# Optimization experiments

Hardware: AMD Instinct MI355X
Metric: run time of the kernel (lower is better)

## Reference

```python
import jax, jax.numpy as jnp
import numpy as np

MU = 0.5
SMALL_MASS_CUTOFF = 1e-10
NP_PART = 2_000_000
W = 8            # linear hex stencil, 2^3 nodes per particle
DIM = 3
NC = 2_097_152   # 128^3 grid cells
NS = 200_000     # selected boundary (level-set) nodes


def setup_inputs() -> dict:
    key = jax.random.key(0)
    k0, k1, k2, k3, k4, k5 = jax.random.split(key, 6)
    mass_stack = jax.random.uniform(k0, (NP_PART,), dtype=jnp.float32)
    shapef_grad_stack = jax.random.normal(k1, (NP_PART, W, DIM), dtype=jnp.float32)
    cnode_ids = jax.random.randint(k2, (NP_PART, W), 0, NC, dtype=jnp.int32)
    node_moment_nt = jax.random.normal(k3, (NC, DIM), dtype=jnp.float32)
    node_mass = jax.random.uniform(k4, (NC,), dtype=jnp.float32)
    id_stack = jnp.arange(NS, dtype=jnp.int32)  # unique selected node ids
    velocity_stack = jax.random.normal(k5, (NS, DIM), dtype=jnp.float32)
    return {
        "mass_stack": mass_stack,
        "shapef_grad_stack": shapef_grad_stack,
        "cnode_ids": cnode_ids,
        "node_moment_nt": node_moment_nt,
        "node_mass": node_mass,
        "id_stack": id_stack,
        "velocity_stack": velocity_stack,
    }


def reference(mass_stack, shapef_grad_stack, cnode_ids, node_moment_nt,
              node_mass, id_stack, velocity_stack):
    dim = velocity_stack.shape[-1]
    nc = node_mass.shape[0]

    # ---- P2G: accumulate mass-weighted shape-function gradients into grid normals
    # normal[c] += shapef_grad[p, w, :dim] * mass[p] for every (p, w) -> c = cnode_ids[p, w]
    contrib = shapef_grad_stack * mass_stack[:, None, None]           # [Np, W, dim]
    normal_stack = jax.ops.segment_sum(contrib.reshape(-1, dim),
                                       cnode_ids.reshape(-1),
                                       num_segments=nc)               # [NC, dim]

    # ---- per selected node friction update (vectorized over NS)
    normal = normal_stack[id_stack]          # [NS, dim]
    moment_nt = node_moment_nt[id_stack]     # [NS, dim]
    mass = node_mass[id_stack]               # [NS]

    valid = mass > SMALL_MASS_CUTOFF
    inv_mass = jnp.where(valid, 1.0 / jnp.where(valid, mass, 1.0), 0.0)
    vel_nt = moment_nt * inv_mass[:, None]   # cond(mass>cutoff, m/mass, 0)

    nnorm = jnp.sqrt(jnp.sum(normal * normal, axis=-1, keepdims=True))
    nrm_ok = valid[:, None] & (nnorm > 0)
    normal_hat = jnp.where(nrm_ok, normal / jnp.where(nnorm > 0, nnorm, 1.0), 0.0)

    delta_vel = vel_nt - velocity_stack                                # [NS, dim]
    dvn = jnp.sum(delta_vel * normal_hat, axis=-1)                     # [NS]

    cross = jnp.cross(delta_vel, normal_hat)                           # [NS, 3]
    cnorm = jnp.sqrt(jnp.sum(cross * cross, axis=-1))                  # [NS]
    omega = jnp.where((cnorm > 0)[:, None],
                      cross / jnp.where(cnorm > 0, cnorm, 1.0)[:, None], 0.0)
    mu_prime = jnp.minimum(MU, cnorm / jnp.where(dvn != 0, dvn, 1.0))  # only used when dvn>0
    tangent = normal_hat + mu_prime[:, None] * jnp.cross(normal_hat, omega)

    apply_fric = (dvn > 0.0)[:, None]
    new_vel_nt = jnp.where(apply_fric, vel_nt - dvn[:, None] * tangent, vel_nt)
    levelset_moment = new_vel_nt * mass[:, None]                       # [NS, dim]

    # ---- scatter-set back into the grid moment field
    return node_moment_nt.at[id_stack].set(levelset_moment)
```

## Files before the change

kernel.cpp:

```cpp
#include <hip/hip_runtime.h>


#define MU_F 0.5f
#define SMALL_MASS_CUTOFF 1e-10f

__global__ void build_mask_kernel(const int* __restrict__ id_stack, int ns,
                                  unsigned int* __restrict__ mask,
                                  float* __restrict__ acc) {
    int i = blockIdx.x * blockDim.x + threadIdx.x;
    if (i >= ns) return;
    int id = id_stack[i];
    atomicOr(&mask[id >> 5], 1u << (id & 31));
    size_t b = (size_t)id * 3;
    acc[b + 0] = 0.0f;
    acc[b + 1] = 0.0f;
    acc[b + 2] = 0.0f;
}

template <int LOG2W>
__global__ void p2g_kernel(const float* __restrict__ mass_stack,
                           const float* __restrict__ grad,
                           const int*   __restrict__ ids,
                           const unsigned int* __restrict__ mask,
                           float* __restrict__ acc,
                           int npairs) {
    int pair = blockIdx.x * blockDim.x + threadIdx.x;
    if (pair >= npairs) return;
    int id = ids[pair];
    unsigned int w = mask[(unsigned)id >> 5];
    if (w & (1u << (id & 31))) {
        float m = mass_stack[pair >> LOG2W];
        const float* g = grad + (size_t)pair * 3;
        float gx = g[0], gy = g[1], gz = g[2];
        size_t b = (size_t)id * 3;
        unsafeAtomicAdd(&acc[b + 0], gx * m);
        unsafeAtomicAdd(&acc[b + 1], gy * m);
        unsafeAtomicAdd(&acc[b + 2], gz * m);
    }
}

__global__ void p2g_kernel_generic(const float* __restrict__ mass_stack,
                                   const float* __restrict__ grad,
                                   const int*   __restrict__ ids,
                                   const unsigned int* __restrict__ mask,
                                   float* __restrict__ acc,
                                   int npairs, int W) {
    int pair = blockIdx.x * blockDim.x + threadIdx.x;
    if (pair >= npairs) return;
    int id = ids[pair];
    unsigned int w = mask[(unsigned)id >> 5];
    if (w & (1u << (id & 31))) {
        float m = mass_stack[pair / W];
        const float* g = grad + (size_t)pair * 3;
        size_t b = (size_t)id * 3;
        unsafeAtomicAdd(&acc[b + 0], g[0] * m);
        unsafeAtomicAdd(&acc[b + 1], g[1] * m);
        unsafeAtomicAdd(&acc[b + 2], g[2] * m);
    }
}

__global__ void friction_kernel(const int*   __restrict__ id_stack,
                                const float* __restrict__ velocity,
                                const float* __restrict__ node_mass,
                                const float* __restrict__ node_moment,
                                const float* __restrict__ acc,
                                float* __restrict__ out,
                                int ns) {
    int i = blockIdx.x * blockDim.x + threadIdx.x;
    if (i >= ns) return;
    int id = id_stack[i];
    size_t b = (size_t)id * 3;

    float nx = acc[b + 0], ny = acc[b + 1], nz = acc[b + 2];
    float mass = node_mass[id];
    float mx = node_moment[b + 0], my = node_moment[b + 1], mz = node_moment[b + 2];

    bool valid = mass > SMALL_MASS_CUTOFF;
    float inv_mass = valid ? 1.0f / mass : 0.0f;
    float vx = mx * inv_mass, vy = my * inv_mass, vz = mz * inv_mass;

    float nn = sqrtf(nx * nx + ny * ny + nz * nz);
    bool ok = valid && (nn > 0.0f);
    float hx = 0.0f, hy = 0.0f, hz = 0.0f;
    if (ok) { float r = 1.0f / nn; hx = nx * r; hy = ny * r; hz = nz * r; }

    size_t vb = (size_t)i * 3;
    float dvx = vx - velocity[vb + 0];
    float dvy = vy - velocity[vb + 1];
    float dvz = vz - velocity[vb + 2];
    float dvn = dvx * hx + dvy * hy + dvz * hz;

    float ox = vx, oy = vy, oz = vz;
    if (dvn > 0.0f) {
        float cx = dvy * hz - dvz * hy;
        float cy = dvz * hx - dvx * hz;
        float cz = dvx * hy - dvy * hx;
        float cn = sqrtf(cx * cx + cy * cy + cz * cz);
        float wx = 0.0f, wy = 0.0f, wz = 0.0f;
        if (cn > 0.0f) { float r = 1.0f / cn; wx = cx * r; wy = cy * r; wz = cz * r; }
        float mu_p = fminf(MU_F, cn / dvn);
        float tx = hx + mu_p * (hy * wz - hz * wy);
        float ty = hy + mu_p * (hz * wx - hx * wz);
        float tz = hz + mu_p * (hx * wy - hy * wx);
        ox = vx - dvn * tx;
        oy = vy - dvn * ty;
        oz = vz - dvn * tz;
    }
    out[b + 0] = ox * mass;
    out[b + 1] = oy * mass;
    out[b + 2] = oz * mass;
}

extern "C" void kernel_launch(void* const* d_in, const int* in_sizes, int n_in,
                              void* d_out, int out_size, void* d_ws, size_t ws_size,
                              hipStream_t stream) {
    const float* mass_stack  = (const float*)d_in[0];
    const float* grad        = (const float*)d_in[1];
    const int*   cnode_ids   = (const int*)d_in[2];
    const float* node_moment = (const float*)d_in[3];
    const float* node_mass   = (const float*)d_in[4];
    const int*   id_stack    = (const int*)d_in[5];
    const float* velocity    = (const float*)d_in[6];
    float* out = (float*)d_out;

    const int np     = in_sizes[0];
    const int npairs = in_sizes[2];
    const int nc     = in_sizes[4];
    const int ns     = in_sizes[5];
    const int W      = npairs / np;

    float* acc = (float*)d_ws;
    unsigned int* mask = (unsigned int*)(acc + (size_t)nc * 3);
    const size_t mask_words = (size_t)(nc + 31) / 32;

    (void)hipMemsetAsync(mask, 0, mask_words * sizeof(unsigned int), stream);

    build_mask_kernel<<<(ns + 255) / 256, 256, 0, stream>>>(id_stack, ns, mask, acc);

    const int blocks = (npairs + 255) / 256;
    if (W == 8) {
        p2g_kernel<3><<<blocks, 256, 0, stream>>>(mass_stack, grad, cnode_ids,
                                                  mask, acc, npairs);
    } else if (W == 4) {
        p2g_kernel<2><<<blocks, 256, 0, stream>>>(mass_stack, grad, cnode_ids,
                                                  mask, acc, npairs);
    } else {
        p2g_kernel_generic<<<blocks, 256, 0, stream>>>(mass_stack, grad, cnode_ids,
                                                       mask, acc, npairs, W);
    }

    (void)hipMemcpyAsync(out, node_moment, (size_t)out_size * sizeof(float),
                         hipMemcpyDeviceToDevice, stream);

    friction_kernel<<<(ns + 255) / 256, 256, 0, stream>>>(id_stack, velocity,
                                                          node_mass, node_moment,
                                                          acc, out, ns);
}
```

Before: 518.9 us.

## Pack fixed-point normals into 64-bit atomics and fuse copy with friction epilogue

Replaces three float atomics per contributing pair with two 64-bit integer atomics on fixed-point, biased values, packing x/y into one word and z plus a count and the selected index into the other. The separate device-to-device copy and the friction kernel are merged into one full-grid epilogue that copies untouched cells and applies the friction update to masked ones. An optional compact slot layout is used when the workspace is too small. Fixed-point quantization at 2^-20 loses precision, and overflow is possible if many large contributions land on one node. The count field is only 8 bits wide, so more than 255 contributions to a node would corrupt the stored index.

```diff
diff --git a/kernel.cpp b/kernel.cpp
--- a/kernel.cpp
+++ b/kernel.cpp
@@ -4,77 +4,88 @@
 #define MU_F 0.5f
 #define SMALL_MASS_CUTOFF 1e-10f
 
+#define FP_SCALE 1048576.0f
+#define FP_INV   9.5367431640625e-07f
+#define FP_BIAS  (1 << 24)
+
+typedef unsigned long long u64;
+typedef unsigned int u32;
+
+template <bool COMPACT>
 __global__ void build_mask_kernel(const int* __restrict__ id_stack, int ns,
-                                  unsigned int* __restrict__ mask,
-                                  float* __restrict__ acc) {
+                                  u32* __restrict__ mask,
+                                  u64* __restrict__ acc,
+                                  u32* __restrict__ inv) {
     int i = blockIdx.x * blockDim.x + threadIdx.x;
     if (i >= ns) return;
     int id = id_stack[i];
-    atomicOr(&mask[id >> 5], 1u << (id & 31));
-    size_t b = (size_t)id * 3;
-    acc[b + 0] = 0.0f;
-    acc[b + 1] = 0.0f;
-    acc[b + 2] = 0.0f;
+    atomicOr(&mask[(u32)id >> 5], 1u << (id & 31));
+    size_t slot = COMPACT ? (size_t)i : (size_t)id;
+    if (COMPACT) inv[id] = (u32)i;
+    acc[2 * slot]     = 0ull;
+    acc[2 * slot + 1] = (u64)(u32)i << 40;
 }
 
-template <int LOG2W>
+template <int LOG2W, bool COMPACT>
 __global__ void p2g_kernel(const float* __restrict__ mass_stack,
                            const float* __restrict__ grad,
                            const int*   __restrict__ ids,
-                           const unsigned int* __restrict__ mask,
-                           float* __restrict__ acc,
-                           int npairs) {
+                           const u32*   __restrict__ mask,
+                           const u32*   __restrict__ inv,
+                           u64* __restrict__ acc,
+                           int npairs, int W) {
     int pair = blockIdx.x * blockDim.x + threadIdx.x;
     if (pair >= npairs) return;
     int id = ids[pair];
-    unsigned int w = mask[(unsigned)id >> 5];
-    if (w & (1u << (id & 31))) {
-        float m = mass_stack[pair >> LOG2W];
+    u32 mword = mask[(u32)id >> 5];
+    if (mword & (1u << (id & 31))) {
+        int pidx = (LOG2W > 0) ? (pair >> LOG2W) : (pair / W);
+        float m = mass_stack[pidx];
         const float* g = grad + (size_t)pair * 3;
-        float gx = g[0], gy = g[1], gz = g[2];
-        size_t b = (size_t)id * 3;
-        unsafeAtomicAdd(&acc[b + 0], gx * m);
-        unsafeAtomicAdd(&acc[b + 1], gy * m);
-        unsafeAtomicAdd(&acc[b + 2], gz * m);
+        int xi = __float2int_rn(g[0] * m * FP_SCALE);
+        int yi = __float2int_rn(g[1] * m * FP_SCALE);
+        int zi = __float2int_rn(g[2] * m * FP_SCALE);
+        u64 a = ((u64)(u32)(yi + FP_BIAS) << 32) | (u32)(xi + FP_BIAS);
+        u64 b = (1ull << 32) | (u32)(zi + FP_BIAS);
+        size_t slot = COMPACT ? (size_t)inv[id] : (size_t)id;
+        atomicAdd(&acc[2 * slot], a);
+        atomicAdd(&acc[2 * slot + 1], b);
     }
 }
 
-__global__ void p2g_kernel_generic(const float* __restrict__ mass_stack,
-                                   const float* __restrict__ grad,
-                                   const int*   __restrict__ ids,
-                                   const unsigned int* __restrict__ mask,
-                                   float* __restrict__ acc,
-                                   int npairs, int W) {
-    int pair = blockIdx.x * blockDim.x + threadIdx.x;
-    if (pair >= npairs) return;
-    int id = ids[pair];
-    unsigned int w = mask[(unsigned)id >> 5];
-    if (w & (1u << (id & 31))) {
-        float m = mass_stack[pair / W];
-        const float* g = grad + (size_t)pair * 3;
-        size_t b = (size_t)id * 3;
-        unsafeAtomicAdd(&acc[b + 0], g[0] * m);
-        unsafeAtomicAdd(&acc[b + 1], g[1] * m);
-        unsafeAtomicAdd(&acc[b + 2], g[2] * m);
+template <bool COMPACT>
+__global__ void epilogue_kernel(const float* __restrict__ node_moment,
+                                const u32*   __restrict__ mask,
+                                const u32*   __restrict__ inv,
+                                const u64*   __restrict__ acc,
+                                const float* __restrict__ node_mass,
+                                const float* __restrict__ velocity,
+                                float* __restrict__ out,
+                                int nc) {
+    int c = blockIdx.x * blockDim.x + threadIdx.x;
+    if (c >= nc) return;
+    size_t b3 = (size_t)c * 3;
+    float mx = node_moment[b3 + 0];
+    float my = node_moment[b3 + 1];
+    float mz = node_moment[b3 + 2];
+
+    u32 mword = mask[(u32)c >> 5];
+    if (!(mword & (1u << (c & 31)))) {
+        out[b3 + 0] = mx; out[b3 + 1] = my; out[b3 + 2] = mz;
+        return;
     }
-}
 
-__global__ void friction_kernel(const int*   __restrict__ id_stack,
-                                const float* __restrict__ velocity,
-                                const float* __restrict__ node_mass,
-                                const float* __restrict__ node_moment,
-                                const float* __restrict__ acc,
-                                float* __restrict__ out,
-                                int ns) {
-    int i = blockIdx.x * blockDim.x + threadIdx.x;
-    if (i >= ns) return;
-    int id = id_stack[i];
-    size_t b = (size_t)id * 3;
+    size_t slot = COMPACT ? (size_t)inv[c] : (size_t)c;
+    u64 a  = acc[2 * slot];
+    u64 bb = acc[2 * slot + 1];
+    u32 cnt = (u32)(bb >> 32) & 0xFFu;
+    int i   = (int)(bb >> 40);
+    long long bias = (long long)cnt * (long long)FP_BIAS;
+    float nx = (float)((long long)(a & 0xFFFFFFFFull) - bias) * FP_INV;
+    float ny = (float)((long long)(a >> 32) - bias) * FP_INV;
+    float nz = (float)((long long)(bb & 0xFFFFFFFFull) - bias) * FP_INV;
 
-    float nx = acc[b + 0], ny = acc[b + 1], nz = acc[b + 2];
-    float mass = node_mass[id];
-    float mx = node_moment[b + 0], my = node_moment[b + 1], mz = node_moment[b + 2];
-
+    float mass = node_mass[c];
     bool valid = mass > SMALL_MASS_CUTOFF;
     float inv_mass = valid ? 1.0f / mass : 0.0f;
     float vx = mx * inv_mass, vy = my * inv_mass, vz = mz * inv_mass;
@@ -106,9 +117,9 @@
         oy = vy - dvn * ty;
         oz = vz - dvn * tz;
     }
-    out[b + 0] = ox * mass;
-    out[b + 1] = oy * mass;
-    out[b + 2] = oz * mass;
+    out[b3 + 0] = ox * mass;
+    out[b3 + 1] = oy * mass;
+    out[b3 + 2] = oz * mass;
 }
 
 extern "C" void kernel_launch(void* const* d_in, const int* in_sizes, int n_in,
@@ -129,30 +140,55 @@
     const int ns     = in_sizes[5];
     const int W      = npairs / np;
 
-    float* acc = (float*)d_ws;
-    unsigned int* mask = (unsigned int*)(acc + (size_t)nc * 3);
     const size_t mask_words = (size_t)(nc + 31) / 32;
 
-    (void)hipMemsetAsync(mask, 0, mask_words * sizeof(unsigned int), stream);
+    const size_t need_full    = (size_t)nc * 16 + mask_words * 4;
+    const bool   compact      = ws_size < need_full;
 
-    build_mask_kernel<<<(ns + 255) / 256, 256, 0, stream>>>(id_stack, ns, mask, acc);
-
-    const int blocks = (npairs + 255) / 256;
-    if (W == 8) {
-        p2g_kernel<3><<<blocks, 256, 0, stream>>>(mass_stack, grad, cnode_ids,
-                                                  mask, acc, npairs);
-    } else if (W == 4) {
-        p2g_kernel<2><<<blocks, 256, 0, stream>>>(mass_stack, grad, cnode_ids,
-                                                  mask, acc, npairs);
+    u64* acc;
+    u32* inv;
+    u32* mask;
+    if (!compact) {
+        acc  = (u64*)d_ws;
+        mask = (u32*)(acc + 2 * (size_t)nc);
+        inv  = nullptr;
     } else {
-        p2g_kernel_generic<<<blocks, 256, 0, stream>>>(mass_stack, grad, cnode_ids,
-                                                       mask, acc, npairs, W);
+        acc  = (u64*)d_ws;
+        inv  = (u32*)(acc + 2 * (size_t)ns);
+        mask = inv + (size_t)nc;
     }
 
-    (void)hipMemcpyAsync(out, node_moment, (size_t)out_size * sizeof(float),
-                         hipMemcpyDeviceToDevice, stream);
+    (void)hipMemsetAsync(mask, 0, mask_words * 4, stream);
 
-    friction_kernel<<<(ns + 255) / 256, 256, 0, stream>>>(id_stack, velocity,
-                                                          node_mass, node_moment,
-                                                          acc, out, ns);
+    const int mb = (ns + 255) / 256;
+    const int pb = (npairs + 255) / 256;
+    const int eb = (nc + 255) / 256;
+
+    if (!compact) {
+        build_mask_kernel<false><<<mb, 256, 0, stream>>>(id_stack, ns, mask, acc, inv);
+        if (W == 8)
+            p2g_kernel<3, false><<<pb, 256, 0, stream>>>(mass_stack, grad, cnode_ids,
+                                                         mask, inv, acc, npairs, W);
+        else if (W == 4)
+            p2g_kernel<2, false><<<pb, 256, 0, stream>>>(mass_stack, grad, cnode_ids,
+                                                         mask, inv, acc, npairs, W);
+        else
+            p2g_kernel<0, false><<<pb, 256, 0, stream>>>(mass_stack, grad, cnode_ids,
+                                                         mask, inv, acc, npairs, W);
+        epilogue_kernel<false><<<eb, 256, 0, stream>>>(node_moment, mask, inv, acc,
+                                                       node_mass, velocity, out, nc);
+    } else {
+        build_mask_kernel<true><<<mb, 256, 0, stream>>>(id_stack, ns, mask, acc, inv);
+        if (W == 8)
+            p2g_kernel<3, true><<<pb, 256, 0, stream>>>(mass_stack, grad, cnode_ids,
+                                                        mask, inv, acc, npairs, W);
+        else if (W == 4)
+            p2g_kernel<2, true><<<pb, 256, 0, stream>>>(mass_stack, grad, cnode_ids,
+                                                        mask, inv, acc, npairs, W);
+        else
+            p2g_kernel<0, true><<<pb, 256, 0, stream>>>(mass_stack, grad, cnode_ids,
+                                                        mask, inv, acc, npairs, W);
+        epilogue_kernel<true><<<eb, 256, 0, stream>>>(node_moment, mask, inv, acc,
+                                                      node_mass, velocity, out, nc);
+    }
 }
```

Result: faster. 460.5 us (-11.2%).
